# Performance work log

Hardware: AMD Instinct MI355X
Metric: run time of the kernel (lower is better)

The kernel has to match this reference:

```python
import jax, jax.numpy as jnp
import numpy as np

B, N, F, H = 8, 256, 512, 256  # batch, nodes (=hidden_dim), feature_dim, hidden_dim


def _pair_scores(x, y, W1a, W1b, b1, W2, b2):
    """sigmoid(MLP(concat(x_i, y_j))) for all pairs, without materializing concat.

    x, y: [B, N, H]. W1a/W1b are the two halves of the Linear(2H -> H) weight.
    Returns [B, N, N].
    """
    a = jnp.einsum('bnh,hk->bnk', x, W1a)          # contribution of row i
    c = jnp.einsum('bnh,hk->bnk', y, W1b)          # contribution of row j
    h = jax.nn.relu(a[:, :, None, :] + c[:, None, :, :] + b1)  # [B,N,N,H]
    s = jnp.einsum('bijh,h->bij', h, W2) + b2
    return jax.nn.sigmoid(s)


def setup_inputs() -> dict:
    key = jax.random.key(0)
    ks = jax.random.split(key, 16)
    sc = 0.02
    return {
        'image_features': jax.random.normal(ks[0], (B, N, F), jnp.float32),
        'text_features': jax.random.normal(ks[1], (B, N, F), jnp.float32),
        # feature_transform: Linear(F->H), ReLU, Linear(H->H)
        'ft_W1': jax.random.normal(ks[2], (F, H), jnp.float32) * sc,
        'ft_b1': jnp.zeros((H,), jnp.float32),
        'ft_W2': jax.random.normal(ks[3], (H, H), jnp.float32) * sc,
        'ft_b2': jnp.zeros((H,), jnp.float32),
        # structure_learning: Linear(2H->H) split into two H x H halves, Linear(H->1)
        'sl_W1a': jax.random.normal(ks[4], (H, H), jnp.float32) * sc,
        'sl_W1b': jax.random.normal(ks[5], (H, H), jnp.float32) * sc,
        'sl_b1': jnp.zeros((H,), jnp.float32),
        'sl_W2': jax.random.normal(ks[6], (H,), jnp.float32) * sc,
        'sl_b2': jnp.zeros((), jnp.float32),
        # causal_net: Linear(2H->H) split, Linear(H->1)
        'cn_W1a': jax.random.normal(ks[7], (H, H), jnp.float32) * sc,
        'cn_W1b': jax.random.normal(ks[8], (H, H), jnp.float32) * sc,
        'cn_b1': jnp.zeros((H,), jnp.float32),
        'cn_W2': jax.random.normal(ks[9], (H,), jnp.float32) * sc,
        'cn_b2': jnp.zeros((), jnp.float32),
    }


def reference(image_features, text_features,
              ft_W1, ft_b1, ft_W2, ft_b2,
              sl_W1a, sl_W1b, sl_b1, sl_W2, sl_b2,
              cn_W1a, cn_W1b, cn_b1, cn_W2, cn_b2):
    # --- StructuralLearning ---
    def feat(x):
        h = jax.nn.relu(jnp.einsum('bnf,fh->bnh', x, ft_W1) + ft_b1)
        return jnp.einsum('bnh,hk->bnk', h, ft_W2) + ft_b2

    img_h = feat(image_features)   # [B,N,H]
    txt_h = feat(text_features)    # [B,N,H]
    structure = _pair_scores(img_h, txt_h, sl_W1a, sl_W1b, sl_b1, sl_W2, sl_b2)  # [B,N,N]

    # --- CausalDiscovery (batched over all node pairs; sigmoid(structure) > 0
    # everywhere so every (i,j) is an edge). DAG cycle removal is a CPU-side
    # networkx post-process and is omitted from the differentiable reference. ---
    causal_matrix = _pair_scores(structure, structure, cn_W1a, cn_W1b, cn_b1, cn_W2, cn_b2)

    # --- verify_causal_invariance ---
    stability = jnp.mean(jnp.abs(causal_matrix - jnp.roll(causal_matrix, 1, axis=0)))
    consistency = jnp.mean(jnp.std(causal_matrix, axis=0, ddof=1))  # torch.std is unbiased
    invariance_score = 1.0 - (stability + consistency) / 2

    return structure, causal_matrix, invariance_score
```

## Files before the change

### kernel.cpp

```cpp
#include <hip/hip_runtime.h>
#include <math.h>

#define B_ 8
#define N_ 256
#define F_ 512
#define H_ 256

typedef __attribute__((ext_vector_type(8))) short short8;
typedef __attribute__((ext_vector_type(4))) float floatx4;
typedef _Float16 h2 __attribute__((ext_vector_type(2)));

__device__ __forceinline__ unsigned int f2bf_bits(float f) {
    unsigned int u = __float_as_uint(f);
    return (u + 0x7fffu + ((u >> 16) & 1u)) >> 16;
}
__device__ __forceinline__ unsigned int pack2bf(float a, float b) {
    return f2bf_bits(a) | (f2bf_bits(b) << 16);
}
__device__ __forceinline__ h2 as_h2(unsigned int u) {
    union { unsigned int u; h2 h; } x; x.u = u; return x.h;
}
__device__ __forceinline__ h2 relu2(h2 t) {
    h2 z; z.x = (_Float16)0; z.y = (_Float16)0;
#if __has_builtin(__builtin_elementwise_max)
    return __builtin_elementwise_max(t, z);
#else
    t.x = t.x > z.x ? t.x : z.x;
    t.y = t.y > z.y ? t.y : z.y;
    return t;
#endif
}
__device__ __forceinline__ float fast_sigmoid(float x) {
    return 1.f / (1.f + __expf(-x));
}

__global__ __launch_bounds__(256) void prep_weights(
    const float* __restrict__ ftW1, const float* __restrict__ ftW2,
    const float* __restrict__ slW1a, const float* __restrict__ slW1b,
    const float* __restrict__ cnW1a, const float* __restrict__ cnW1b,
    const float* __restrict__ ftb2, const float* __restrict__ slb1,
    unsigned short* __restrict__ wt, float* __restrict__ bA, float* __restrict__ bB,
    float* __restrict__ accum)
{
    if (blockIdx.x == 0 && threadIdx.x < 4) accum[threadIdx.x] = 0.f;

    if (blockIdx.x >= 224) {
        const int second = (blockIdx.x == 225);
        const float* W = second ? slW1b : slW1a;
        const int n = threadIdx.x;
        float s0 = 0.f, s1 = 0.f, s2 = 0.f, s3 = 0.f;
#pragma unroll 4
        for (int k = 0; k < 256; k += 4) {
            s0 = fmaf(ftb2[k],     W[(k)     * 256 + n], s0);
            s1 = fmaf(ftb2[k + 1], W[(k + 1) * 256 + n], s1);
            s2 = fmaf(ftb2[k + 2], W[(k + 2) * 256 + n], s2);
            s3 = fmaf(ftb2[k + 3], W[(k + 3) * 256 + n], s3);
        }
        float s = (s0 + s1) + (s2 + s3);
        if (second) bB[n] = s + slb1[n];
        else        bA[n] = s;
        return;
    }

    int t = blockIdx.x * 256 + threadIdx.x;
    if (t < 49152) {
        const float* src; int K; unsigned short* dst;
        if (t < 16384) { src = ftW1; K = 512; dst = wt; }
        else {
            int m  = (t - 16384) >> 13;
            t = (t - 16384) & 8191; K = 256;
            switch (m) {
                case 0:  src = slW1a; dst = wt + 131072; break;
                case 1:  src = slW1b; dst = wt + 196608; break;
                case 2:  src = cnW1a; dst = wt + 262144; break;
                default: src = cnW1b; dst = wt + 327680; break;
            }
        }
        const int n  = t & 255;
        const int k0 = (t >> 8) * 8;
        unsigned int p[4];
#pragma unroll
        for (int j = 0; j < 4; ++j) {
            float f0 = src[(size_t)(k0 + 2 * j)     * 256 + n];
            float f1 = src[(size_t)(k0 + 2 * j + 1) * 256 + n];
            p[j] = pack2bf(f0, f1);
        }
        *(uint4*)(dst + (size_t)n * K + k0) = make_uint4(p[0], p[1], p[2], p[3]);
    } else {
        const int lt = t - 49152;
        const int k  = lt >> 5;
        const int n0 = (lt & 31) * 8;
        const float* src = ftW2 + (size_t)k * 256 + n0;
        float4 f0 = *(const float4*)(src);
        float4 f1 = *(const float4*)(src + 4);
        unsigned short* dst = wt + 393216 + (size_t)k * 256 + n0;
        *(uint4*)dst = make_uint4(pack2bf(f0.x, f0.y), pack2bf(f0.z, f0.w),
                                  pack2bf(f1.x, f1.y), pack2bf(f1.z, f1.w));
    }
}

struct GJob {
    const void* A0; const void* A1; int aSplitBlk; int aBf16;
    const unsigned short* Wt0; const unsigned short* Wt1;
    const float* bias0; const float* bias1;
    int wRowSplitBlk; int wColSplitBlk;
    void* out; int outMode; int ldOut; int K; int relu;
};

__global__ __launch_bounds__(256) void gemm_mfma(GJob j0, GJob j1, int j0By)
{
    __shared__ unsigned short As[2][64][40];
    __shared__ unsigned short Bs[2][64][40];

    const bool firstJob = ((int)blockIdx.y < j0By);
    const GJob j = firstJob ? j0 : j1;
    const int by = firstJob ? blockIdx.y : blockIdx.y - j0By;
    const int bx = blockIdx.x;
    const int tid = threadIdx.x;
    const int K = j.K;

    const void* Abase; int arow0;
    if (by < j.aSplitBlk) { Abase = j.A0; arow0 = by * 64; }
    else                  { Abase = j.A1; arow0 = (by - j.aSplitBlk) * 64; }

    int wcolBlk = bx;
    bool second;
    if (j.wColSplitBlk > 0) {
        second = (bx >= j.wColSplitBlk);
        if (second) wcolBlk = bx - j.wColSplitBlk;
    } else {
        second = (by >= j.wRowSplitBlk);
    }
    const unsigned short* Wt = second ? j.Wt1 : j.Wt0;
    const float* bias        = second ? j.bias1 : j.bias0;
    const int wcol = wcolBlk * 64;

    const int r    = tid >> 2;
    const int kq   = (tid & 3) * 8;
    const int lane = tid & 63;
    const int wv   = tid >> 6;
    const int col  = lane & 15;
    const int quad = lane >> 4;

    floatx4 acc[4] = {};

    uint4 apack, bpack;
    float4 af0, af1;
    const unsigned short* Abf = (const unsigned short*)Abase + (size_t)(arow0 + r) * K + kq;
    const float*          Afp = (const float*)Abase + (size_t)(arow0 + r) * K + kq;
    const unsigned short* Wp  = Wt + (size_t)(wcol + r) * K + kq;

    if (j.aBf16) apack = *(const uint4*)(Abf);
    else { af0 = *(const float4*)(Afp); af1 = *(const float4*)(Afp + 4); }
    bpack = *(const uint4*)(Wp);

    int p = 0;
    for (int k0 = 0; k0 < K; k0 += 32) {
        uint4 aw;
        if (j.aBf16) aw = apack;
        else aw = make_uint4(pack2bf(af0.x, af0.y), pack2bf(af0.z, af0.w),
                             pack2bf(af1.x, af1.y), pack2bf(af1.z, af1.w));
        uint4 bw = bpack;

        *(uint4*)&As[p][r][kq] = aw;
        *(uint4*)&Bs[p][r][kq] = bw;

        if (k0 + 32 < K) {
            if (j.aBf16) apack = *(const uint4*)(Abf + k0 + 32);
            else {
                af0 = *(const float4*)(Afp + k0 + 32);
                af1 = *(const float4*)(Afp + k0 + 32 + 4);
            }
            bpack = *(const uint4*)(Wp + k0 + 32);
        }

        __syncthreads();

        short8 bfrag = *(const short8*)&Bs[p][wv * 16 + col][quad * 8];
#pragma unroll
        for (int tm = 0; tm < 4; ++tm) {
            short8 afrag = *(const short8*)&As[p][tm * 16 + col][quad * 8];
            acc[tm] = __builtin_amdgcn_mfma_f32_16x16x32_bf16(afrag, bfrag, acc[tm], 0, 0, 0);
        }
        p ^= 1;
    }

    const int ocol = bx * 64 + wv * 16 + col;
    const int bcol = wcol + wv * 16 + col;
    const float bv = bias ? bias[bcol] : 0.f;
#pragma unroll
    for (int tm = 0; tm < 4; ++tm) {
#pragma unroll
        for (int rr = 0; rr < 4; ++rr) {
            float v = acc[tm][rr] + bv;
            if (j.relu) v = fmaxf(v, 0.f);
            const size_t o = (size_t)(by * 64 + tm * 16 + quad * 4 + rr) * j.ldOut + ocol;
            if (j.outMode == 0)      ((float*)j.out)[o] = v;
            else if (j.outMode == 1) ((unsigned short*)j.out)[o] = (unsigned short)f2bf_bits(v);
            else                     ((_Float16*)j.out)[o] = (_Float16)v;
        }
    }
}

__global__ __launch_bounds__(256) void pair_score(
    const unsigned short* __restrict__ Abase, int ldA,
    const unsigned short* __restrict__ Cbase, int ldC,
    const float* __restrict__ W2, const float* __restrict__ b2p,
    float* __restrict__ out)
{
    __shared__ unsigned short aS[64][256];
    __shared__ unsigned short cS[32][256];

    const int tid = threadIdx.x;
    const int b   = blockIdx.z;
    const int i0b = blockIdx.y * 64;
    const int j0b = blockIdx.x * 32;

    {
        const int rr = tid >> 3;
        const int c8 = tid & 7;
#pragma unroll
        for (int rep = 0; rep < 8; ++rep) {
            const int li = rr + 32 * (rep & 1);
            const int ch = c8 + 8 * (rep >> 1);
            uint4 v = *(const uint4*)(Abase + ((size_t)b * N_ + i0b + li) * ldA + ch * 8);
            *(uint4*)&aS[li][(ch ^ ((li >> 1) & 7)) * 8] = v;
        }
#pragma unroll
        for (int rep = 0; rep < 4; ++rep) {
            const int ch = c8 + 8 * rep;
            uint4 v = *(const uint4*)(Cbase + ((size_t)b * N_ + j0b + rr) * ldC + ch * 8);
            *(uint4*)&cS[rr][(ch ^ ((rr >> 1) & 7)) * 8] = v;
        }
    }
    __syncthreads();

    const int ti = tid >> 4, tj = tid & 15;
    const int ia = ti * 4, jc = tj * 2;
    const int k01 = (2 * ti) & 7;
    const int k23 = (2 * ti + 1) & 7;
    const int kc  = tj & 7;

    float s[4][2] = {};

#pragma unroll 4
    for (int ch = 0; ch < 32; ++ch) {
        const uint4 a0 = *(const uint4*)&aS[ia    ][(ch ^ k01) * 8];
        const uint4 a1 = *(const uint4*)&aS[ia + 1][(ch ^ k01) * 8];
        const uint4 a2 = *(const uint4*)&aS[ia + 2][(ch ^ k23) * 8];
        const uint4 a3 = *(const uint4*)&aS[ia + 3][(ch ^ k23) * 8];
        const uint4 c0 = *(const uint4*)&cS[jc    ][(ch ^ kc) * 8];
        const uint4 c1 = *(const uint4*)&cS[jc + 1][(ch ^ kc) * 8];
        const float* w = &W2[ch * 8];
#pragma unroll
        for (int u = 0; u < 4; ++u) {
            const float w0 = w[2 * u], w1 = w[2 * u + 1];
            const h2 hc0 = as_h2(((const unsigned int*)&c0)[u]);
            const h2 hc1 = as_h2(((const unsigned int*)&c1)[u]);
#define ACC2(su, ha, hc) { h2 t_ = relu2((ha) + (hc)); \
    su = fmaf((float)t_.x, w0, su); su = fmaf((float)t_.y, w1, su); }
            {
                const h2 ha = as_h2(((const unsigned int*)&a0)[u]);
                ACC2(s[0][0], ha, hc0); ACC2(s[0][1], ha, hc1);
            }
            {
                const h2 ha = as_h2(((const unsigned int*)&a1)[u]);
                ACC2(s[1][0], ha, hc0); ACC2(s[1][1], ha, hc1);
            }
            {
                const h2 ha = as_h2(((const unsigned int*)&a2)[u]);
                ACC2(s[2][0], ha, hc0); ACC2(s[2][1], ha, hc1);
            }
            {
                const h2 ha = as_h2(((const unsigned int*)&a3)[u]);
                ACC2(s[3][0], ha, hc0); ACC2(s[3][1], ha, hc1);
            }
#undef ACC2
        }
    }

    const float bb = b2p[0];
#pragma unroll
    for (int rr = 0; rr < 4; ++rr) {
        float2 o;
        o.x = fast_sigmoid(s[rr][0] + bb);
        o.y = fast_sigmoid(s[rr][1] + bb);
        *(float2*)&out[((size_t)b * N_ + i0b + ia + rr) * N_ + j0b + jc] = o;
    }
}

__global__ __launch_bounds__(256) void invariance_partial(
    const float* __restrict__ causal, float* __restrict__ accum,
    float* __restrict__ out_scalar)
{
    const int idx = blockIdx.x * 256 + threadIdx.x;
    float x[B_];
#pragma unroll
    for (int b = 0; b < B_; ++b) x[b] = causal[(size_t)b * (N_ * N_) + idx];

    float stab = 0.f, mean = 0.f;
#pragma unroll
    for (int b = 0; b < B_; ++b) {
        stab += fabsf(x[b] - x[(b + B_ - 1) % B_]);
        mean += x[b];
    }
    mean *= (1.f / B_);
    float var = 0.f;
#pragma unroll
    for (int b = 0; b < B_; ++b) {
        float d = x[b] - mean;
        var = fmaf(d, d, var);
    }
    float sd = sqrtf(var * (1.f / (B_ - 1)));

#pragma unroll
    for (int off = 32; off > 0; off >>= 1) {
        stab += __shfl_down(stab, off, 64);
        sd   += __shfl_down(sd, off, 64);
    }

    __shared__ float red[8];
    if ((threadIdx.x & 63) == 0) {
        red[threadIdx.x >> 6]       = stab;
        red[4 + (threadIdx.x >> 6)] = sd;
    }
    __syncthreads();
    if (threadIdx.x == 0) {
        float s = (red[0] + red[1]) + (red[2] + red[3]);
        float d = (red[4] + red[5]) + (red[6] + red[7]);
        atomicAdd(&accum[0], s);
        atomicAdd(&accum[1], d);
        __threadfence();
        unsigned int prev = atomicAdd((unsigned int*)&accum[2], 1u);
        if (prev == 255u) {
            float st  = atomicAdd(&accum[0], 0.f);
            float sdt = atomicAdd(&accum[1], 0.f);
            float stability   = st  * (1.f / (float)(B_ * N_ * N_));
            float consistency = sdt * (1.f / (float)(N_ * N_));
            out_scalar[0] = 1.f - (stability + consistency) * 0.5f;
        }
    }
}

extern "C" void kernel_launch(void* const* d_in, const int* in_sizes, int n_in,
                              void* d_out, int out_size, void* d_ws, size_t ws_size,
                              hipStream_t stream)
{
    const float* img   = (const float*)d_in[0];
    const float* txt   = (const float*)d_in[1];
    const float* ftW1  = (const float*)d_in[2];
    const float* ftb1  = (const float*)d_in[3];
    const float* ftW2  = (const float*)d_in[4];
    const float* ftb2  = (const float*)d_in[5];
    const float* slW1a = (const float*)d_in[6];
    const float* slW1b = (const float*)d_in[7];
    const float* slb1  = (const float*)d_in[8];
    const float* slW2  = (const float*)d_in[9];
    const float* slb2  = (const float*)d_in[10];
    const float* cnW1a = (const float*)d_in[11];
    const float* cnW1b = (const float*)d_in[12];
    const float* cnb1  = (const float*)d_in[13];
    const float* cnW2  = (const float*)d_in[14];
    const float* cnb2  = (const float*)d_in[15];

    float* out       = (float*)d_out;
    float* structure = out;
    float* causal    = out + (size_t)B_ * N_ * N_;
    float* inv       = out + 2 * (size_t)B_ * N_ * N_;

    unsigned short* wt     = (unsigned short*)d_ws;
    unsigned short* wcombT = wt + 458752;
    float* bA    = (float*)(wt + 589824);
    float* bB    = bA + 256;
    float* accum = bA + 512;
    unsigned short* h1b  = wt + 655360;
    unsigned short* acb  = wt + 1703936;
    unsigned short* ac2b = acb;

    dim3 blk(256);
    const int BIG = 1 << 20;

    const unsigned short* wtFT1 = wt;
    const unsigned short* wtSLA = wt + 131072;
    const unsigned short* wtSLB = wt + 196608;
    const unsigned short* wtCNA = wt + 262144;
    const unsigned short* wtCNB = wt + 327680;
    const unsigned short* ftW2r = wt + 393216;

    prep_weights<<<dim3(226), blk, 0, stream>>>(
        ftW1, ftW2, slW1a, slW1b, cnW1a, cnW1b, ftb2, slb1, wt, bA, bB, accum);

    {
        GJob g1  = { img, txt, 32, 0, wtFT1, wtFT1, ftb1, ftb1, BIG, 0,
                     h1b, 1, 256, 512, 1 };
        GJob wcb = { wtSLA, wtSLB, 4, 1, ftW2r, ftW2r, nullptr, nullptr, BIG, 0,
                     wcombT, 1, 256, 256, 0 };
        gemm_mfma<<<dim3(4, 72), blk, 0, stream>>>(g1, wcb, 64);
    }

    {
        GJob g2 = { h1b, h1b, BIG, 1, wcombT, wcombT + 65536, bA, bB, 32, 0,
                    acb, 2, 256, 256, 0 };
        gemm_mfma<<<dim3(4, 64), blk, 0, stream>>>(g2, g2, 64);
    }

    pair_score<<<dim3(8, 4, 8), blk, 0, stream>>>(
        acb, 256, acb + (size_t)2048 * 256, 256, slW2, slb2, structure);

    {
        GJob g4 = { structure, structure, BIG, 0, wtCNA, wtCNB, nullptr, cnb1, BIG, 4,
                    ac2b, 2, 512, 256, 0 };
        gemm_mfma<<<dim3(8, 32), blk, 0, stream>>>(g4, g4, 32);
    }

    pair_score<<<dim3(8, 4, 8), blk, 0, stream>>>(
        ac2b, 512, ac2b + 256, 512, cnW2, cnb2, causal);

    invariance_partial<<<dim3(N_ * N_ / 256), blk, 0, stream>>>(causal, accum, inv);
}
```

Measured before the change: 164.1 us.

## Drop weight-prep kernel by converting fp32 weights to bf16 inside GEMM loads

Removes the separate prep_weights launch. The GEMM operand loader now reads fp32 weights directly, either row-major or strided transposed, and converts them to bf16 while staging into shared memory. The bias-folding and accumulator-zeroing work moves into special blocks of the first GEMM launch, which gets an extra grid row. This saves one kernel launch and the round trip through the workspace, at the cost of strided, uncoalesced 4-byte transposed loads and repeated fp32-to-bf16 conversion in every block that uses the weights.

```diff
diff --git a/kernel.cpp b/kernel.cpp
--- a/kernel.cpp
+++ b/kernel.cpp
@@ -34,87 +34,79 @@
     return 1.f / (1.f + __expf(-x));
 }
 
-__global__ __launch_bounds__(256) void prep_weights(
-    const float* __restrict__ ftW1, const float* __restrict__ ftW2,
-    const float* __restrict__ slW1a, const float* __restrict__ slW1b,
-    const float* __restrict__ cnW1a, const float* __restrict__ cnW1b,
-    const float* __restrict__ ftb2, const float* __restrict__ slb1,
-    unsigned short* __restrict__ wt, float* __restrict__ bA, float* __restrict__ bB,
-    float* __restrict__ accum)
-{
-    if (blockIdx.x == 0 && threadIdx.x < 4) accum[threadIdx.x] = 0.f;
-
-    if (blockIdx.x >= 224) {
-        const int second = (blockIdx.x == 225);
-        const float* W = second ? slW1b : slW1a;
-        const int n = threadIdx.x;
-        float s0 = 0.f, s1 = 0.f, s2 = 0.f, s3 = 0.f;
-#pragma unroll 4
-        for (int k = 0; k < 256; k += 4) {
-            s0 = fmaf(ftb2[k],     W[(k)     * 256 + n], s0);
-            s1 = fmaf(ftb2[k + 1], W[(k + 1) * 256 + n], s1);
-            s2 = fmaf(ftb2[k + 2], W[(k + 2) * 256 + n], s2);
-            s3 = fmaf(ftb2[k + 3], W[(k + 3) * 256 + n], s3);
-        }
-        float s = (s0 + s1) + (s2 + s3);
-        if (second) bB[n] = s + slb1[n];
-        else        bA[n] = s;
-        return;
-    }
-
-    int t = blockIdx.x * 256 + threadIdx.x;
-    if (t < 49152) {
-        const float* src; int K; unsigned short* dst;
-        if (t < 16384) { src = ftW1; K = 512; dst = wt; }
-        else {
-            int m  = (t - 16384) >> 13;
-            t = (t - 16384) & 8191; K = 256;
-            switch (m) {
-                case 0:  src = slW1a; dst = wt + 131072; break;
-                case 1:  src = slW1b; dst = wt + 196608; break;
-                case 2:  src = cnW1a; dst = wt + 262144; break;
-                default: src = cnW1b; dst = wt + 327680; break;
-            }
-        }
-        const int n  = t & 255;
-        const int k0 = (t >> 8) * 8;
-        unsigned int p[4];
-#pragma unroll
-        for (int j = 0; j < 4; ++j) {
-            float f0 = src[(size_t)(k0 + 2 * j)     * 256 + n];
-            float f1 = src[(size_t)(k0 + 2 * j + 1) * 256 + n];
-            p[j] = pack2bf(f0, f1);
-        }
-        *(uint4*)(dst + (size_t)n * K + k0) = make_uint4(p[0], p[1], p[2], p[3]);
-    } else {
-        const int lt = t - 49152;
-        const int k  = lt >> 5;
-        const int n0 = (lt & 31) * 8;
-        const float* src = ftW2 + (size_t)k * 256 + n0;
-        float4 f0 = *(const float4*)(src);
-        float4 f1 = *(const float4*)(src + 4);
-        unsigned short* dst = wt + 393216 + (size_t)k * 256 + n0;
-        *(uint4*)dst = make_uint4(pack2bf(f0.x, f0.y), pack2bf(f0.z, f0.w),
-                                  pack2bf(f1.x, f1.y), pack2bf(f1.z, f1.w));
-    }
-}
-
 struct GJob {
-    const void* A0; const void* A1; int aSplitBlk; int aBf16;
-    const unsigned short* Wt0; const unsigned short* Wt1;
+    const void* A0; const void* A1; int aSplitBlk; int aMode; int ldA;
+    const void* B0; const void* B1; int bMode; int ldB;
     const float* bias0; const float* bias1;
     int wRowSplitBlk; int wColSplitBlk;
     void* out; int outMode; int ldOut; int K; int relu;
 };
 
-__global__ __launch_bounds__(256) void gemm_mfma(GJob j0, GJob j1, int j0By)
+struct SpecP {
+    const float* slW1a; const float* slW1b; const float* ftb2; const float* slb1;
+    float* bA; float* bB; float* accum;
+};
+
+struct Pref { uint4 u; float4 f0, f1; float fs[8]; };
+
+__device__ __forceinline__ void op_load(Pref& P, int mode, const void* base,
+                                        int ld, int row, int k)
+{
+    if (mode == 0) {
+        P.u = *(const uint4*)((const unsigned short*)base + (size_t)row * ld + k);
+    } else if (mode == 1) {
+        const float* s = (const float*)base + (size_t)row * ld + k;
+        P.f0 = *(const float4*)s;
+        P.f1 = *(const float4*)(s + 4);
+    } else {
+        const float* s = (const float*)base + (size_t)k * ld + row;
+#pragma unroll
+        for (int jj = 0; jj < 8; ++jj) P.fs[jj] = s[(size_t)jj * ld];
+    }
+}
+__device__ __forceinline__ uint4 to_bf(const Pref& P, int mode)
+{
+    if (mode == 0) return P.u;
+    if (mode == 1) return make_uint4(pack2bf(P.f0.x, P.f0.y), pack2bf(P.f0.z, P.f0.w),
+                                     pack2bf(P.f1.x, P.f1.y), pack2bf(P.f1.z, P.f1.w));
+    return make_uint4(pack2bf(P.fs[0], P.fs[1]), pack2bf(P.fs[2], P.fs[3]),
+                      pack2bf(P.fs[4], P.fs[5]), pack2bf(P.fs[6], P.fs[7]));
+}
+
+__device__ void special_block(const SpecP& sp, int bx)
+{
+    const int tid = threadIdx.x;
+    if (bx == 2) { if (tid < 4) sp.accum[tid] = 0.f; return; }
+    if (bx > 2) return;
+    const float* W = bx ? sp.slW1b : sp.slW1a;
+    const int n = tid;
+    float s[16];
+#pragma unroll
+    for (int u = 0; u < 16; ++u) s[u] = 0.f;
+    for (int k0 = 0; k0 < 256; k0 += 16) {
+#pragma unroll
+        for (int u = 0; u < 16; ++u)
+            s[u] = fmaf(sp.ftb2[k0 + u], W[(size_t)(k0 + u) * 256 + n], s[u]);
+    }
+    float t = 0.f;
+#pragma unroll
+    for (int u = 0; u < 16; ++u) t += s[u];
+    if (bx) sp.bB[n] = t + sp.slb1[n];
+    else    sp.bA[n] = t;
+}
+
+__global__ __launch_bounds__(256) void gemm_mfma(GJob j0, GJob j1, int j1By,
+                                                 int spBy, SpecP sp)
 {
     __shared__ unsigned short As[2][64][40];
     __shared__ unsigned short Bs[2][64][40];
 
-    const bool firstJob = ((int)blockIdx.y < j0By);
-    const GJob j = firstJob ? j0 : j1;
-    const int by = firstJob ? blockIdx.y : blockIdx.y - j0By;
+    const int byG = blockIdx.x == blockIdx.x ? (int)blockIdx.y : 0;
+    if (byG == spBy) { special_block(sp, blockIdx.x); return; }
+
+    const bool isJ1 = byG < j1By;
+    const GJob j = isJ1 ? j1 : j0;
+    const int by = isJ1 ? byG : byG - j1By - (spBy >= 0 ? 1 : 0);
     const int bx = blockIdx.x;
     const int tid = threadIdx.x;
     const int K = j.K;
@@ -131,8 +123,8 @@
     } else {
         second = (by >= j.wRowSplitBlk);
     }
-    const unsigned short* Wt = second ? j.Wt1 : j.Wt0;
-    const float* bias        = second ? j.bias1 : j.bias0;
+    const void* Bbase     = second ? j.B1 : j.B0;
+    const float* bias     = second ? j.bias1 : j.bias0;
     const int wcol = wcolBlk * 64;
 
     const int r    = tid >> 2;
@@ -144,34 +136,21 @@
 
     floatx4 acc[4] = {};
 
-    uint4 apack, bpack;
-    float4 af0, af1;
-    const unsigned short* Abf = (const unsigned short*)Abase + (size_t)(arow0 + r) * K + kq;
-    const float*          Afp = (const float*)Abase + (size_t)(arow0 + r) * K + kq;
-    const unsigned short* Wp  = Wt + (size_t)(wcol + r) * K + kq;
-
-    if (j.aBf16) apack = *(const uint4*)(Abf);
-    else { af0 = *(const float4*)(Afp); af1 = *(const float4*)(Afp + 4); }
-    bpack = *(const uint4*)(Wp);
+    Pref PA, PB;
+    op_load(PA, j.aMode, Abase, j.ldA, arow0 + r, kq);
+    op_load(PB, j.bMode, Bbase, j.ldB, wcol + r, kq);
 
     int p = 0;
     for (int k0 = 0; k0 < K; k0 += 32) {
-        uint4 aw;
-        if (j.aBf16) aw = apack;
-        else aw = make_uint4(pack2bf(af0.x, af0.y), pack2bf(af0.z, af0.w),
-                             pack2bf(af1.x, af1.y), pack2bf(af1.z, af1.w));
-        uint4 bw = bpack;
+        uint4 aw = to_bf(PA, j.aMode);
+        uint4 bw = to_bf(PB, j.bMode);
 
         *(uint4*)&As[p][r][kq] = aw;
         *(uint4*)&Bs[p][r][kq] = bw;
 
         if (k0 + 32 < K) {
-            if (j.aBf16) apack = *(const uint4*)(Abf + k0 + 32);
-            else {
-                af0 = *(const float4*)(Afp + k0 + 32);
-                af1 = *(const float4*)(Afp + k0 + 32 + 4);
-            }
-            bpack = *(const uint4*)(Wp + k0 + 32);
+            op_load(PA, j.aMode, Abase, j.ldA, arow0 + r, k0 + 32 + kq);
+            op_load(PB, j.bMode, Bbase, j.ldB, wcol + r, k0 + 32 + kq);
         }
 
         __syncthreads();
@@ -368,49 +347,41 @@
     float* causal    = out + (size_t)B_ * N_ * N_;
     float* inv       = out + 2 * (size_t)B_ * N_ * N_;
 
-    unsigned short* wt     = (unsigned short*)d_ws;
-    unsigned short* wcombT = wt + 458752;
-    float* bA    = (float*)(wt + 589824);
+    unsigned short* wcombT = (unsigned short*)d_ws;
+    float* bA    = (float*)(wcombT + 131072);
     float* bB    = bA + 256;
     float* accum = bA + 512;
-    unsigned short* h1b  = wt + 655360;
-    unsigned short* acb  = wt + 1703936;
+    unsigned short* h1b  = wcombT + 135168;
+    unsigned short* acb  = wcombT + 1183744;
     unsigned short* ac2b = acb;
 
     dim3 blk(256);
     const int BIG = 1 << 20;
 
-    const unsigned short* wtFT1 = wt;
-    const unsigned short* wtSLA = wt + 131072;
-    const unsigned short* wtSLB = wt + 196608;
-    const unsigned short* wtCNA = wt + 262144;
-    const unsigned short* wtCNB = wt + 327680;
-    const unsigned short* ftW2r = wt + 393216;
-
-    prep_weights<<<dim3(226), blk, 0, stream>>>(
-        ftW1, ftW2, slW1a, slW1b, cnW1a, cnW1b, ftb2, slb1, wt, bA, bB, accum);
+    SpecP sp = { slW1a, slW1b, ftb2, slb1, bA, bB, accum };
+    SpecP spNull = {};
 
     {
-        GJob g1  = { img, txt, 32, 0, wtFT1, wtFT1, ftb1, ftb1, BIG, 0,
-                     h1b, 1, 256, 512, 1 };
-        GJob wcb = { wtSLA, wtSLB, 4, 1, ftW2r, ftW2r, nullptr, nullptr, BIG, 0,
-                     wcombT, 1, 256, 256, 0 };
-        gemm_mfma<<<dim3(4, 72), blk, 0, stream>>>(g1, wcb, 64);
+        GJob g1  = { img, txt, 32, 1, 512,  ftW1, ftW1, 2, 256,
+                     ftb1, ftb1, BIG, 0,  h1b, 1, 256, 512, 1 };
+        GJob wcb = { slW1a, slW1b, 4, 2, 256,  ftW2, ftW2, 1, 256,
+                     nullptr, nullptr, BIG, 0,  wcombT, 1, 256, 256, 0 };
+        gemm_mfma<<<dim3(4, 73), blk, 0, stream>>>(g1, wcb, 8, 8, sp);
     }
 
     {
-        GJob g2 = { h1b, h1b, BIG, 1, wcombT, wcombT + 65536, bA, bB, 32, 0,
-                    acb, 2, 256, 256, 0 };
-        gemm_mfma<<<dim3(4, 64), blk, 0, stream>>>(g2, g2, 64);
+        GJob g2 = { h1b, h1b, BIG, 0, 256,  wcombT, wcombT + 65536, 0, 256,
+                    bA, bB, 32, 0,  acb, 2, 256, 256, 0 };
+        gemm_mfma<<<dim3(4, 64), blk, 0, stream>>>(g2, g2, 0, -1, spNull);
     }
 
     pair_score<<<dim3(8, 4, 8), blk, 0, stream>>>(
         acb, 256, acb + (size_t)2048 * 256, 256, slW2, slb2, structure);
 
     {
-        GJob g4 = { structure, structure, BIG, 0, wtCNA, wtCNB, nullptr, cnb1, BIG, 4,
-                    ac2b, 2, 512, 256, 0 };
-        gemm_mfma<<<dim3(8, 32), blk, 0, stream>>>(g4, g4, 32);
+        GJob g4 = { structure, structure, BIG, 1, 256,  cnW1a, cnW1b, 2, 256,
+                    nullptr, cnb1, BIG, 4,  ac2b, 2, 512, 256, 0 };
+        gemm_mfma<<<dim3(8, 32), blk, 0, stream>>>(g4, g4, 0, -1, spNull);
     }
 
     pair_score<<<dim3(8, 4, 8), blk, 0, stream>>>(
```

Measured after the change: 176.1 us. 7.3% more time.
